# Performance work log

Hardware: AMD Instinct MI355X
Metric: run time of the kernel (lower is better)

Reference implementation:

```python
import jax, jax.numpy as jnp
import numpy as np

N_NODES = 500_000
N_EDGES = 8_000_000
W_PDE, W_BC, W_J1, W_J2 = 1.0, 100.0, 10.0, 10.0
EPS = 1e-8


def setup_inputs() -> dict:
    key = jax.random.key(0)
    ks = jax.random.split(key, 12)
    inp = {
        "u_pred": jax.random.normal(ks[0], (N_NODES, 1), jnp.float32),
        "x": jax.random.normal(ks[1], (N_NODES, 4), jnp.float32),
        # positions in [-1, 1] so the |pos|>0.99 boundary mask is nonempty
        "pos": 2.0 * jax.random.uniform(ks[2], (N_NODES, 2), jnp.float32) - 1.0,
        "y": jax.random.normal(ks[3], (N_NODES, 1), jnp.float32),
        "source": jax.random.normal(ks[4], (N_NODES, 1), jnp.float32),
        "j1": jax.random.normal(ks[5], (N_NODES, 1), jnp.float32),
        "coeff_dx": jax.random.normal(ks[6], (N_EDGES,), jnp.float32),
        "coeff_dy": jax.random.normal(ks[7], (N_EDGES,), jnp.float32),
        "coeff_lap": jax.random.normal(ks[8], (N_EDGES,), jnp.float32),
        "a": jnp.array([0.8], jnp.float32),
        "b": jnp.array([0.6], jnp.float32),
        "c": jnp.array([0.5], jnp.float32),
        "beta_minus": jnp.array([1.0], jnp.float32),
        "beta_plus": jnp.array([10.0], jnp.float32),
        "edge_index": jax.random.randint(ks[9], (2, N_EDGES), 0, N_NODES, jnp.int32),
        "edge_attr": jax.random.randint(ks[10], (N_EDGES,), 0, 2, jnp.int32),
    }
    return inp


def _masked_mean(sq, mask):
    # mean of sq over entries where mask is True (count>=1 guard, jit-safe)
    cnt = jnp.maximum(jnp.sum(mask.astype(sq.dtype)), 1.0)
    return jnp.sum(jnp.where(mask[:, None], sq, 0.0)) / cnt


def reference(u_pred, x, pos, y, source, j1, coeff_dx, coeff_dy, coeff_lap,
              a, b, c, beta_minus, beta_plus, edge_index, edge_attr):
    N = u_pred.shape[0]
    row, col = edge_index[0], edge_index[1]
    # GFD stencil derivatives: scatter-add of weighted differences over edges
    u_diff = u_pred[col] - u_pred[row]                       # [E,1]
    dx = jax.ops.segment_sum(u_diff * coeff_dx[:, None], row, num_segments=N)
    dy = jax.ops.segment_sum(u_diff * coeff_dy[:, None], row, num_segments=N)
    lap = jax.ops.segment_sum(u_diff * coeff_lap[:, None], row, num_segments=N)

    z = x[:, 3:4]                                            # [N,1]
    beta = jnp.where(z < 0, beta_minus, beta_plus)           # [N,1]
    res_pde = -lap - source / beta
    loss_pde = jnp.mean(res_pde ** 2)

    mask_bnd = (jnp.abs(pos[:, 0]) > 0.99) | (jnp.abs(pos[:, 1]) > 0.99)  # [N]
    loss_bc = _masked_mean((u_pred - y) ** 2, mask_bnd)

    # Interface (heterogeneous) edges
    m_het = edge_attr == 1                                   # [E]
    src, dst = row, col
    sign = jnp.sign(z[dst])                                  # [E,1]
    val_jump_pred = sign * (u_pred[dst] - u_pred[src])
    loss_j1 = _masked_mean((val_jump_pred - j1[src]) ** 2, m_het)

    # Elliptic interface normal at edge midpoints
    pos_mid = 0.5 * (pos[src] + pos[dst])                    # [E,2]
    nx = pos_mid[:, 0] / a ** 2
    ny = pos_mid[:, 1] / b ** 2
    nrm = jnp.maximum(jnp.sqrt(nx ** 2 + ny ** 2), EPS)      # [E]
    nxu, nyu = (nx / nrm)[:, None], (ny / nrm)[:, None]
    dn_src = dx[src] * nxu + dy[src] * nyu
    dn_dst = dx[dst] * nxu + dy[dst] * nyu
    flux_jump_pred = sign * (beta[dst] * dn_dst - beta[src] * dn_src)
    target_j2 = (2.0 * nrm * (c * beta_plus - beta_minus))[:, None]
    loss_j2 = _masked_mean((flux_jump_pred - target_j2) ** 2, m_het)

    loss_jump = W_J1 * loss_j1 + W_J2 * loss_j2
    total_loss = W_PDE * loss_pde + W_BC * loss_bc + loss_jump
    return total_loss
```

## Files before the change

kernel.cpp:

```cpp
#include <hip/hip_runtime.h>
#include <hip/hip_fp16.h>

#define N_NODES 500000
#define N_EDGES 8000000
#define EPSF 1e-8f

#define WIN_SHIFT 11
#define WINDOW 2048
#define NB 245
#define CHUNK 2000
#define NQ (CHUNK / 4)
#define NCHUNK 4000
#define SC_ITEMS 16

typedef int            v4i __attribute__((ext_vector_type(4)));
typedef float          v4f __attribute__((ext_vector_type(4)));
typedef unsigned short v4h __attribute__((ext_vector_type(4)));
typedef int            v2i __attribute__((ext_vector_type(2)));

struct Accum { double pde_sum, bc_sum, bc_cnt, j1_sum, j2_sum, het_cnt; };

__device__ __forceinline__ unsigned short f2h(float f) {
    return __half_as_ushort(__float2half(f));
}
__device__ __forceinline__ float h2f(unsigned short u) {
    return __half2float(__ushort_as_half(u));
}

__device__ double block_reduce(double v) {
    __shared__ double sm[16];
    __syncthreads();
    for (int off = 32; off; off >>= 1) v += __shfl_down(v, off, 64);
    const int lane = threadIdx.x & 63, wid = threadIdx.x >> 6;
    if (lane == 0) sm[wid] = v;
    __syncthreads();
    if (wid == 0) {
        const int nw = blockDim.x >> 6;
        v = (lane < nw) ? sm[lane] : 0.0;
        for (int off = 8; off; off >>= 1) v += __shfl_down(v, off, 64);
    }
    return v;
}

__device__ unsigned int block_excl_scan_u32(unsigned int x, unsigned int* smw) {
    const int lane = threadIdx.x & 63, wid = threadIdx.x >> 6;
    unsigned int v = x;
    for (int d = 1; d < 64; d <<= 1) {
        unsigned int t = __shfl_up(v, d, 64);
        if (lane >= d) v += t;
    }
    if (lane == 63) smw[wid] = v;
    __syncthreads();
    unsigned int base = 0;
    for (int w = 0; w < wid; ++w) base += smw[w];
    return base + v - x;
}

__global__ void prep(const float* __restrict__ x, const float* __restrict__ u,
                     const float* __restrict__ j1,
                     unsigned int* __restrict__ Tsrc, unsigned int* __restrict__ Tdst,
                     unsigned short* __restrict__ szh) {
    const int stride = gridDim.x * blockDim.x;
    for (int i = blockIdx.x * blockDim.x + threadIdx.x; i < N_NODES; i += stride) {
        const float z = x[4 * i + 3];
        const unsigned int uhb = f2h(u[i]);
        const unsigned short sb = f2h((float)(z > 0.f) - (float)(z < 0.f));
        Tsrc[i] = uhb | ((unsigned int)f2h(j1[i]) << 16);
        Tdst[i] = uhb | ((unsigned int)sb << 16);
        szh[i]  = sb;
    }
}

__global__ void k_hist(const v4i* __restrict__ row4, const v4i* __restrict__ attr4,
                       unsigned int* __restrict__ histC,
                       unsigned int* __restrict__ hist_het) {
    __shared__ unsigned int h[NB];
    __shared__ unsigned int hh;
    for (int i = threadIdx.x; i < NB; i += blockDim.x) h[i] = 0;
    if (threadIdx.x == 0) hh = 0;
    __syncthreads();
    const int ch = blockIdx.x;
    unsigned int my = 0;
    for (int q = threadIdx.x; q < NQ; q += blockDim.x) {
        const v4i r = __builtin_nontemporal_load(&row4[ch * NQ + q]);
        const v4i a = __builtin_nontemporal_load(&attr4[ch * NQ + q]);
        atomicAdd(&h[r[0] >> WIN_SHIFT], 1u);
        atomicAdd(&h[r[1] >> WIN_SHIFT], 1u);
        atomicAdd(&h[r[2] >> WIN_SHIFT], 1u);
        atomicAdd(&h[r[3] >> WIN_SHIFT], 1u);
        my += (a[0] == 1) + (a[1] == 1) + (a[2] == 1) + (a[3] == 1);
    }
    if (my) atomicAdd(&hh, my);
    __syncthreads();
    for (int i = threadIdx.x; i < NB; i += blockDim.x)
        histC[(size_t)ch * NB + i] = h[i];
    if (threadIdx.x == 0) hist_het[ch] = hh;
}

__global__ void k_scan1(const unsigned int* __restrict__ histC,
                        unsigned int* __restrict__ scannedB,
                        unsigned int* __restrict__ total) {
    __shared__ unsigned int v[NCHUNK];
    __shared__ unsigned int smw[4];
    const int b = blockIdx.x;
    for (int i = threadIdx.x; i < NCHUNK; i += blockDim.x)
        v[i] = histC[(size_t)i * NB + b];
    __syncthreads();
    const int i0 = threadIdx.x * SC_ITEMS;
    unsigned int s = 0;
    for (int k = 0; k < SC_ITEMS; ++k) { const int i = i0 + k; if (i < NCHUNK) s += v[i]; }
    const unsigned int ex = block_excl_scan_u32(s, smw);
    if (threadIdx.x == blockDim.x - 1) {
        total[b] = ex + s;
        scannedB[(size_t)b * (NCHUNK + 1) + NCHUNK] = ex + s;
    }
    unsigned int run = ex;
    for (int k = 0; k < SC_ITEMS; ++k) {
        const int i = i0 + k;
        if (i < NCHUNK) { scannedB[(size_t)b * (NCHUNK + 1) + i] = run; run += v[i]; }
    }
}

__global__ void k_scanhet(const unsigned int* __restrict__ hist_het,
                          unsigned int* __restrict__ hetbase) {
    __shared__ unsigned int v[NCHUNK];
    __shared__ unsigned int smw[4];
    for (int i = threadIdx.x; i < NCHUNK; i += blockDim.x) v[i] = hist_het[i];
    __syncthreads();
    const int i0 = threadIdx.x * SC_ITEMS;
    unsigned int s = 0;
    for (int k = 0; k < SC_ITEMS; ++k) { const int i = i0 + k; if (i < NCHUNK) s += v[i]; }
    const unsigned int ex = block_excl_scan_u32(s, smw);
    if (threadIdx.x == blockDim.x - 1) hetbase[NCHUNK] = ex + s;
    unsigned int run = ex;
    for (int k = 0; k < SC_ITEMS; ++k) {
        const int i = i0 + k;
        if (i < NCHUNK) { hetbase[i] = run; run += v[i]; }
    }
}

__global__ void k_tr(const unsigned int* __restrict__ in, unsigned int* __restrict__ out) {
    __shared__ unsigned int t[32][33];
    const int ch0 = blockIdx.x * 32, b0 = blockIdx.y * 32;
    const int tx = threadIdx.x & 31, ty0 = threadIdx.x >> 5;
    for (int j = ty0; j < 32; j += 8) {
        const int b = b0 + j, ch = ch0 + tx;
        if (b < NB && ch < NCHUNK + 1) t[j][tx] = in[(size_t)b * (NCHUNK + 1) + ch];
    }
    __syncthreads();
    for (int j = ty0; j < 32; j += 8) {
        const int ch = ch0 + j, b = b0 + tx;
        if (ch < NCHUNK + 1 && b < NB) out[(size_t)ch * NB + b] = t[tx][j];
    }
}

__global__ void k_scan2(const unsigned int* __restrict__ total, unsigned int* __restrict__ baseb) {
    __shared__ unsigned int smw[4];
    const unsigned int x = (threadIdx.x < NB) ? total[threadIdx.x] : 0;
    const unsigned int ex = block_excl_scan_u32(x, smw);
    if (threadIdx.x < NB) baseb[threadIdx.x] = ex;
}

template<int EMIT_HET>
__global__ void __launch_bounds__(256, 7)
k_scatter(const v4i* __restrict__ row4, const v4i* __restrict__ col4,
          const v4i* __restrict__ attr4,
          const v4f* __restrict__ cdx4, const v4f* __restrict__ cdy4,
          const v4f* __restrict__ clap4,
          const unsigned int* __restrict__ Tsrc, const unsigned int* __restrict__ Tdst,
          const unsigned int* __restrict__ baseb,
          const unsigned int* __restrict__ scannedC,
          const unsigned int* __restrict__ hetbase,
          v4h* __restrict__ rec, v2i* __restrict__ het, Accum* __restrict__ acc) {
    __shared__ int           lcur[NB];
    __shared__ unsigned int  lbase[NB];
    __shared__ unsigned int  gdest[NB];
    __shared__ unsigned int  smw[4];
    __shared__ v4h           o4[CHUNK];
    __shared__ unsigned char obk[CHUNK];
    __shared__ int           hcur;

    const int ch = blockIdx.x;
    unsigned int cnt = 0;
    if (threadIdx.x < NB) {
        const unsigned int s0 = scannedC[(size_t)ch * NB + threadIdx.x];
        const unsigned int s1 = scannedC[(size_t)(ch + 1) * NB + threadIdx.x];
        cnt = s1 - s0;
        gdest[threadIdx.x] = baseb[threadIdx.x] + s0;
        lcur[threadIdx.x] = 0;
    }
    if (EMIT_HET && threadIdx.x == 0) hcur = (int)hetbase[ch];
    const unsigned int exv = block_excl_scan_u32(cnt, smw);
    if (threadIdx.x < NB) lbase[threadIdx.x] = exv;
    __syncthreads();

    double j1s = 0.0;
    int hc = 0;
    for (int q = threadIdx.x; q < NQ; q += blockDim.x) {
        const v4i r4 = __builtin_nontemporal_load(&row4[ch * NQ + q]);
        const v4i c4 = __builtin_nontemporal_load(&col4[ch * NQ + q]);
        const v4i a4 = __builtin_nontemporal_load(&attr4[ch * NQ + q]);
        const v4f cx = __builtin_nontemporal_load(&cdx4[ch * NQ + q]);
        const v4f cy = __builtin_nontemporal_load(&cdy4[ch * NQ + q]);
        const v4f cl = __builtin_nontemporal_load(&clap4[ch * NQ + q]);
#pragma unroll
        for (int k = 0; k < 4; ++k) {
            const int r = r4[k], c = c4[k];
            const unsigned int ts = Tsrc[r];
            const unsigned int td = Tdst[c];
            const float ud = h2f((unsigned short)td) - h2f((unsigned short)ts);
            const int b = r >> WIN_SHIFT;
            const int p = (int)lbase[b] + atomicAdd(&lcur[b], 1);
            v4h rc;
            rc[0] = (unsigned short)(r & (WINDOW - 1));
            rc[1] = f2h(ud * cx[k]);
            rc[2] = f2h(ud * cy[k]);
            rc[3] = f2h(ud * cl[k]);
            o4[p] = rc;
            obk[p] = (unsigned char)b;
            if (a4[k] == 1) {
                const float d = h2f((unsigned short)(td >> 16)) * ud -
                                h2f((unsigned short)(ts >> 16));
                j1s += (double)(d * d);
                hc++;
                if (EMIT_HET) {
                    const int pos = atomicAdd(&hcur, 1);
                    v2i e; e[0] = r; e[1] = c;
                    __builtin_nontemporal_store(e, &het[pos]);
                }
            }
        }
    }
    __syncthreads();

    for (int i = threadIdx.x; i < CHUNK; i += blockDim.x) {
        const v4h rc = o4[i];
        const int b = obk[i];
        const unsigned int dest = gdest[b] + (unsigned int)(i - (int)lbase[b]);
        __builtin_nontemporal_store(rc, &rec[dest]);
    }

    double t = block_reduce(j1s);
    if (threadIdx.x == 0) atomicAdd(&acc->j1_sum, t);
    t = block_reduce((double)hc);
    if (threadIdx.x == 0) atomicAdd(&acc->het_cnt, t);
}

__global__ void k_acc(const v4h* __restrict__ rec,
                      const unsigned int* __restrict__ baseb,
                      const unsigned int* __restrict__ total,
                      const float* __restrict__ u, const unsigned short* __restrict__ szh,
                      const float2* __restrict__ pos2,
                      const float* __restrict__ y, const float* __restrict__ source,
                      const float* __restrict__ a_p, const float* __restrict__ b_p,
                      const float* __restrict__ bm_p, const float* __restrict__ bp_p,
                      v4h* __restrict__ Q, Accum* __restrict__ acc) {
    __shared__ float a3[WINDOW * 3];
    for (int i = threadIdx.x; i < WINDOW * 3; i += blockDim.x) a3[i] = 0.f;
    __syncthreads();
    const int b = blockIdx.x;
    const int s = (int)baseb[b];
    const int e = s + (int)total[b];
    for (int i = s + threadIdx.x; i < e; i += blockDim.x) {
        const v4h rc = __builtin_nontemporal_load(&rec[i]);
        const int lr = (int)(rc[0] & (WINDOW - 1)) * 3;
        atomicAdd(&a3[lr + 0], h2f(rc[1]));
        atomicAdd(&a3[lr + 1], h2f(rc[2]));
        atomicAdd(&a3[lr + 2], h2f(rc[3]));
    }
    __syncthreads();
    const float av = a_p[0], bv = b_p[0], bm = bm_p[0], bp = bp_p[0];
    const float ha = 0.5f / (av * av), hb = 0.5f / (bv * bv);
    double pde = 0.0, bcs = 0.0;
    int bcc = 0;
    const int n0 = b << WIN_SHIFT;
    const int n1 = min(n0 + WINDOW, N_NODES);
    for (int i = n0 + threadIdx.x; i < n1; i += blockDim.x) {
        const int l = (i - n0) * 3;
        const float szv = h2f(szh[i]);
        const float beta = (szv < 0.f) ? bm : bp;
        const float2 p = pos2[i];
        v4h qo;
        qo[0] = f2h(p.x * ha);
        qo[1] = f2h(p.y * hb);
        qo[2] = (unsigned short)((f2h(beta * a3[l]) & 0xFFFEu) | (szv < 0.f ? 1u : 0u));
        qo[3] = (unsigned short)((f2h(beta * a3[l + 1]) & 0xFFFEu) | (szv == 0.f ? 1u : 0u));
        Q[i] = qo;
        const float res = -a3[l + 2] - source[i] / beta;
        pde += (double)(res * res);
        if (fabsf(p.x) > 0.99f || fabsf(p.y) > 0.99f) {
            const float d = u[i] - y[i];
            bcs += (double)(d * d);
            bcc++;
        }
    }
    double t = block_reduce(pde);
    if (threadIdx.x == 0) atomicAdd(&acc->pde_sum, t);
    t = block_reduce(bcs);
    if (threadIdx.x == 0) atomicAdd(&acc->bc_sum, t);
    t = block_reduce((double)bcc);
    if (threadIdx.x == 0) atomicAdd(&acc->bc_cnt, t);
}

__global__ void k_pass2c(const v2i* __restrict__ het,
                         const unsigned int* __restrict__ hetbase,
                         const v4h* __restrict__ Q,
                         const float* __restrict__ c_p,
                         const float* __restrict__ bm_p, const float* __restrict__ bp_p,
                         Accum* __restrict__ acc) {
    const float tgt = 2.f * (c_p[0] * bp_p[0] - bm_p[0]);
    const int tot = (int)hetbase[NCHUNK];
    double j2s = 0.0;
    const int stride = gridDim.x * blockDim.x;
    for (int i = blockIdx.x * blockDim.x + threadIdx.x; i < tot; i += stride) {
        const v2i e = __builtin_nontemporal_load(&het[i]);
        const v4h qr = Q[e[0]];
        const v4h qc = Q[e[1]];
        const float nx = h2f(qr[0]) + h2f(qc[0]);
        const float ny = h2f(qr[1]) + h2f(qc[1]);
        const float nrm = fmaxf(sqrtf(nx * nx + ny * ny), EPSF);
        const float B = ((h2f(qc[2]) - h2f(qr[2])) * nx +
                         (h2f(qc[3]) - h2f(qr[3])) * ny) / nrm;
        const float sz = (qc[3] & 1u) ? 0.f : ((qc[2] & 1u) ? -1.f : 1.f);
        const float d = sz * B - tgt * nrm;
        j2s += (double)(d * d);
    }
    const double t = block_reduce(j2s);
    if (threadIdx.x == 0) atomicAdd(&acc->j2_sum, t);
}

__global__ void k_pass2(const v4i* __restrict__ row4, const v4i* __restrict__ col4,
                        const v4i* __restrict__ attr4,
                        const v4h* __restrict__ Q, const unsigned short* __restrict__ szh,
                        const float* __restrict__ c_p,
                        const float* __restrict__ bm_p, const float* __restrict__ bp_p,
                        Accum* __restrict__ acc) {
    const float tgt = 2.f * (c_p[0] * bp_p[0] - bm_p[0]);
    double j2s = 0.0;
    const int stride = gridDim.x * blockDim.x;
    const int NQT = N_EDGES / 4;
    for (int q = blockIdx.x * blockDim.x + threadIdx.x; q < NQT; q += stride) {
        const v4i r4 = __builtin_nontemporal_load(&row4[q]);
        const v4i c4 = __builtin_nontemporal_load(&col4[q]);
        const v4i a4 = __builtin_nontemporal_load(&attr4[q]);
#pragma unroll
        for (int k = 0; k < 4; ++k) {
            if (a4[k] != 1) continue;
            const int r = r4[k], c = c4[k];
            const v4h qr = Q[r];
            const v4h qc = Q[c];
            const float nx = h2f(qr[0]) + h2f(qc[0]);
            const float ny = h2f(qr[1]) + h2f(qc[1]);
            const float nrm = fmaxf(sqrtf(nx * nx + ny * ny), EPSF);
            const float B = ((h2f(qc[2]) - h2f(qr[2])) * nx +
                             (h2f(qc[3]) - h2f(qr[3])) * ny) / nrm;
            const float d = h2f(szh[c]) * B - tgt * nrm;
            j2s += (double)(d * d);
        }
    }
    const double t = block_reduce(j2s);
    if (threadIdx.x == 0) atomicAdd(&acc->j2_sum, t);
}

__global__ void fb_edge1(const unsigned int* __restrict__ Tsrc,
                         const unsigned int* __restrict__ Tdst,
                         const float* __restrict__ cdx, const float* __restrict__ cdy,
                         const float* __restrict__ clap,
                         const int* __restrict__ row, const int* __restrict__ col,
                         const int* __restrict__ attr,
                         float* __restrict__ rep, Accum* __restrict__ acc) {
    double j1s = 0.0;
    int hc = 0;
    const int stride = gridDim.x * blockDim.x;
    for (int e = blockIdx.x * blockDim.x + threadIdx.x; e < N_EDGES; e += stride) {
        const int r = row[e], c = col[e];
        const unsigned int ts = Tsrc[r];
        const unsigned int td = Tdst[c];
        const float ud = h2f((unsigned short)td) - h2f((unsigned short)ts);
        atomicAdd(&rep[4 * (size_t)r + 0], ud * cdx[e]);
        atomicAdd(&rep[4 * (size_t)r + 1], ud * cdy[e]);
        atomicAdd(&rep[4 * (size_t)r + 2], ud * clap[e]);
        if (attr[e] == 1) {
            const float d = h2f((unsigned short)(td >> 16)) * ud -
                            h2f((unsigned short)(ts >> 16));
            j1s += (double)(d * d);
            hc++;
        }
    }
    double t = block_reduce(j1s);
    if (threadIdx.x == 0) atomicAdd(&acc->j1_sum, t);
    t = block_reduce((double)hc);
    if (threadIdx.x == 0) atomicAdd(&acc->het_cnt, t);
}

__global__ void fb_reduce(const float4* __restrict__ rep,
                          const float* __restrict__ u, const unsigned short* __restrict__ szh,
                          const float2* __restrict__ pos2,
                          const float* __restrict__ y, const float* __restrict__ source,
                          const float* __restrict__ a_p, const float* __restrict__ b_p,
                          const float* __restrict__ bm_p, const float* __restrict__ bp_p,
                          v4h* __restrict__ Q, Accum* __restrict__ acc) {
    const float av = a_p[0], bv = b_p[0], bm = bm_p[0], bp = bp_p[0];
    const float ha = 0.5f / (av * av), hb = 0.5f / (bv * bv);
    double pde = 0.0, bcs = 0.0;
    int bcc = 0;
    const int stride = gridDim.x * blockDim.x;
    for (int i = blockIdx.x * blockDim.x + threadIdx.x; i < N_NODES; i += stride) {
        const float4 v = rep[i];
        const float szv = h2f(szh[i]);
        const float beta = (szv < 0.f) ? bm : bp;
        const float2 p = pos2[i];
        v4h qo;
        qo[0] = f2h(p.x * ha);
        qo[1] = f2h(p.y * hb);
        qo[2] = (unsigned short)((f2h(beta * v.x) & 0xFFFEu) | (szv < 0.f ? 1u : 0u));
        qo[3] = (unsigned short)((f2h(beta * v.y) & 0xFFFEu) | (szv == 0.f ? 1u : 0u));
        Q[i] = qo;
        const float res = -v.z - source[i] / beta;
        pde += (double)(res * res);
        if (fabsf(p.x) > 0.99f || fabsf(p.y) > 0.99f) {
            const float d = u[i] - y[i];
            bcs += (double)(d * d);
            bcc++;
        }
    }
    double t = block_reduce(pde);
    if (threadIdx.x == 0) atomicAdd(&acc->pde_sum, t);
    t = block_reduce(bcs);
    if (threadIdx.x == 0) atomicAdd(&acc->bc_sum, t);
    t = block_reduce((double)bcc);
    if (threadIdx.x == 0) atomicAdd(&acc->bc_cnt, t);
}

__global__ void finalize(const Accum* __restrict__ acc, float* __restrict__ out) {
    if (threadIdx.x == 0 && blockIdx.x == 0) {
        const double loss_pde = acc->pde_sum / (double)N_NODES;
        const double loss_bc  = acc->bc_sum / fmax(acc->bc_cnt, 1.0);
        const double hc       = fmax(acc->het_cnt, 1.0);
        out[0] = (float)(loss_pde + 100.0 * loss_bc +
                         10.0 * (acc->j1_sum / hc) + 10.0 * (acc->j2_sum / hc));
    }
}

extern "C" void kernel_launch(void* const* d_in, const int* in_sizes, int n_in,
                              void* d_out, int out_size, void* d_ws, size_t ws_size,
                              hipStream_t stream) {
    const float* u_pred = (const float*)d_in[0];
    const float* x      = (const float*)d_in[1];
    const float2* pos2  = (const float2*)d_in[2];
    const float* y      = (const float*)d_in[3];
    const float* source = (const float*)d_in[4];
    const float* j1v    = (const float*)d_in[5];
    const float* cdx    = (const float*)d_in[6];
    const float* cdy    = (const float*)d_in[7];
    const float* clap   = (const float*)d_in[8];
    const float* a_p    = (const float*)d_in[9];
    const float* b_p    = (const float*)d_in[10];
    const float* c_p    = (const float*)d_in[11];
    const float* bm_p   = (const float*)d_in[12];
    const float* bp_p   = (const float*)d_in[13];
    const int* row_idx  = (const int*)d_in[14];
    const int* col_idx  = row_idx + N_EDGES;
    const int* eattr    = (const int*)d_in[15];

    char* base_p = (char*)d_ws;
    size_t off = 0;
    auto alloc = [&](size_t bytes) { void* p = base_p + off; off = (off + bytes + 63) & ~(size_t)63; return p; };

    Accum* acc = (Accum*)alloc(sizeof(Accum));
    unsigned int* Tsrc = (unsigned int*)alloc((size_t)N_NODES * 4);
    unsigned int* Tdst = (unsigned int*)alloc((size_t)N_NODES * 4);
    unsigned short* szh = (unsigned short*)alloc((size_t)N_NODES * 2);
    v4h* Q = (v4h*)alloc((size_t)N_NODES * 8);
    unsigned int* histC    = (unsigned int*)alloc((size_t)(NCHUNK + 1) * NB * 4);
    unsigned int* scannedB = (unsigned int*)alloc((size_t)NB * (NCHUNK + 1) * 4);
    unsigned int* total    = (unsigned int*)alloc(NB * 4);
    unsigned int* baseb    = (unsigned int*)alloc(NB * 4);
    unsigned int* hist_het = (unsigned int*)alloc((size_t)NCHUNK * 4);
    unsigned int* hetbase  = (unsigned int*)alloc((size_t)(NCHUNK + 1) * 4);
    unsigned int* scannedC = histC;
    const size_t misc_end = off;
    v4h* rec = (v4h*)alloc((size_t)N_EDGES * 8);
    const size_t need_sort = off;
    v2i* het = (v2i*)alloc((size_t)N_EDGES * 8);
    const size_t need_het = off;

    const int threads = 256;
    const int nblocks = (N_NODES + threads - 1) / threads;

    hipMemsetAsync(d_ws, 0, 64, stream);
    prep<<<nblocks, threads, 0, stream>>>(x, u_pred, j1v, Tsrc, Tdst, szh);

    if (ws_size >= need_sort) {
        const bool emit = (ws_size >= need_het);
        k_hist<<<NCHUNK, threads, 0, stream>>>((const v4i*)row_idx, (const v4i*)eattr,
                                               histC, hist_het);
        k_scan1<<<NB, threads, 0, stream>>>(histC, scannedB, total);
        k_scanhet<<<1, threads, 0, stream>>>(hist_het, hetbase);
        {
            dim3 g((NCHUNK + 1 + 31) / 32, (NB + 31) / 32);
            k_tr<<<g, 256, 0, stream>>>(scannedB, scannedC);
        }
        k_scan2<<<1, threads, 0, stream>>>(total, baseb);
        if (emit) {
            k_scatter<1><<<NCHUNK, threads, 0, stream>>>(
                (const v4i*)row_idx, (const v4i*)col_idx, (const v4i*)eattr,
                (const v4f*)cdx, (const v4f*)cdy, (const v4f*)clap,
                Tsrc, Tdst, baseb, scannedC, hetbase, rec, het, acc);
        } else {
            k_scatter<0><<<NCHUNK, threads, 0, stream>>>(
                (const v4i*)row_idx, (const v4i*)col_idx, (const v4i*)eattr,
                (const v4f*)cdx, (const v4f*)cdy, (const v4f*)clap,
                Tsrc, Tdst, baseb, scannedC, hetbase, rec, het, acc);
        }
        k_acc<<<NB, threads, 0, stream>>>(rec, baseb, total, u_pred, szh, pos2, y, source,
                                          a_p, b_p, bm_p, bp_p, Q, acc);
        if (emit) {
            k_pass2c<<<1024, threads, 0, stream>>>(het, hetbase, Q, c_p, bm_p, bp_p, acc);
        } else {
            k_pass2<<<2048, threads, 0, stream>>>((const v4i*)row_idx, (const v4i*)col_idx,
                                                  (const v4i*)eattr, Q, szh,
                                                  c_p, bm_p, bp_p, acc);
        }
    } else {
        float4* rep = (float4*)(base_p + misc_end);
        hipMemsetAsync(rep, 0, (size_t)N_NODES * 16, stream);
        fb_edge1<<<2048, threads, 0, stream>>>(Tsrc, Tdst, cdx, cdy, clap,
                                               row_idx, col_idx, eattr, (float*)rep, acc);
        fb_reduce<<<nblocks, threads, 0, stream>>>(rep, u_pred, szh, pos2, y, source,
                                                   a_p, b_p, bm_p, bp_p, Q, acc);
        k_pass2<<<2048, threads, 0, stream>>>((const v4i*)row_idx, (const v4i*)col_idx,
                                              (const v4i*)eattr, Q, szh,
                                              c_p, bm_p, bp_p, acc);
    }

    finalize<<<1, 64, 0, stream>>>(acc, (float*)d_out);
}
```

Measured before the change: 429.3 us.

## Defer row-side gather and j1 loss to windowed accumulate kernel via LDS

```diff
diff --git a/kernel.cpp b/kernel.cpp
--- a/kernel.cpp
+++ b/kernel.cpp
@@ -57,17 +57,13 @@
 }
 
 __global__ void prep(const float* __restrict__ x, const float* __restrict__ u,
-                     const float* __restrict__ j1,
-                     unsigned int* __restrict__ Tsrc, unsigned int* __restrict__ Tdst,
-                     unsigned short* __restrict__ szh) {
+                     unsigned int* __restrict__ G, unsigned short* __restrict__ szh) {
     const int stride = gridDim.x * blockDim.x;
     for (int i = blockIdx.x * blockDim.x + threadIdx.x; i < N_NODES; i += stride) {
         const float z = x[4 * i + 3];
-        const unsigned int uhb = f2h(u[i]);
-        const unsigned short sb = f2h((float)(z > 0.f) - (float)(z < 0.f));
-        Tsrc[i] = uhb | ((unsigned int)f2h(j1[i]) << 16);
-        Tdst[i] = uhb | ((unsigned int)sb << 16);
-        szh[i]  = sb;
+        const unsigned int sz2 = (z < 0.f) ? 1u : ((z > 0.f) ? 0u : 2u);
+        G[i] = (unsigned int)f2h(u[i]) | (sz2 << 16);
+        szh[i] = f2h((float)(z > 0.f) - (float)(z < 0.f));
     }
 }
 
@@ -162,21 +158,23 @@
 }
 
 template<int EMIT_HET>
-__global__ void __launch_bounds__(256, 7)
+__global__ void __launch_bounds__(256, 6)
 k_scatter(const v4i* __restrict__ row4, const v4i* __restrict__ col4,
           const v4i* __restrict__ attr4,
           const v4f* __restrict__ cdx4, const v4f* __restrict__ cdy4,
           const v4f* __restrict__ clap4,
-          const unsigned int* __restrict__ Tsrc, const unsigned int* __restrict__ Tdst,
+          const unsigned int* __restrict__ G,
           const unsigned int* __restrict__ baseb,
           const unsigned int* __restrict__ scannedC,
           const unsigned int* __restrict__ hetbase,
-          v4h* __restrict__ rec, v2i* __restrict__ het, Accum* __restrict__ acc) {
+          v4h* __restrict__ rec8, unsigned short* __restrict__ recl,
+          v2i* __restrict__ het) {
     __shared__ int           lcur[NB];
     __shared__ unsigned int  lbase[NB];
     __shared__ unsigned int  gdest[NB];
     __shared__ unsigned int  smw[4];
     __shared__ v4h           o4[CHUNK];
+    __shared__ unsigned short oclap[CHUNK];
     __shared__ unsigned char obk[CHUNK];
     __shared__ int           hcur;
 
@@ -194,8 +192,6 @@
     if (threadIdx.x < NB) lbase[threadIdx.x] = exv;
     __syncthreads();
 
-    double j1s = 0.0;
-    int hc = 0;
     for (int q = threadIdx.x; q < NQ; q += blockDim.x) {
         const v4i r4 = __builtin_nontemporal_load(&row4[ch * NQ + q]);
         const v4i c4 = __builtin_nontemporal_load(&col4[ch * NQ + q]);
@@ -206,75 +202,87 @@
 #pragma unroll
         for (int k = 0; k < 4; ++k) {
             const int r = r4[k], c = c4[k];
-            const unsigned int ts = Tsrc[r];
-            const unsigned int td = Tdst[c];
-            const float ud = h2f((unsigned short)td) - h2f((unsigned short)ts);
+            const unsigned int g = G[c];
+            const unsigned int isHet = (a4[k] == 1) ? 1u : 0u;
             const int b = r >> WIN_SHIFT;
             const int p = (int)lbase[b] + atomicAdd(&lcur[b], 1);
             v4h rc;
-            rc[0] = (unsigned short)(r & (WINDOW - 1));
-            rc[1] = f2h(ud * cx[k]);
-            rc[2] = f2h(ud * cy[k]);
-            rc[3] = f2h(ud * cl[k]);
+            rc[0] = (unsigned short)((r & (WINDOW - 1)) | ((g >> 16) << 11) | (isHet << 13));
+            rc[1] = (unsigned short)(g & 0xFFFFu);
+            rc[2] = f2h(cx[k]);
+            rc[3] = f2h(cy[k]);
             o4[p] = rc;
+            oclap[p] = f2h(cl[k]);
             obk[p] = (unsigned char)b;
-            if (a4[k] == 1) {
-                const float d = h2f((unsigned short)(td >> 16)) * ud -
-                                h2f((unsigned short)(ts >> 16));
-                j1s += (double)(d * d);
-                hc++;
-                if (EMIT_HET) {
-                    const int pos = atomicAdd(&hcur, 1);
-                    v2i e; e[0] = r; e[1] = c;
-                    __builtin_nontemporal_store(e, &het[pos]);
-                }
+            if (EMIT_HET && isHet) {
+                const int pos = atomicAdd(&hcur, 1);
+                v2i e; e[0] = r; e[1] = c;
+                __builtin_nontemporal_store(e, &het[pos]);
             }
         }
     }
     __syncthreads();
 
     for (int i = threadIdx.x; i < CHUNK; i += blockDim.x) {
-        const v4h rc = o4[i];
         const int b = obk[i];
         const unsigned int dest = gdest[b] + (unsigned int)(i - (int)lbase[b]);
-        __builtin_nontemporal_store(rc, &rec[dest]);
-    }
-
-    double t = block_reduce(j1s);
-    if (threadIdx.x == 0) atomicAdd(&acc->j1_sum, t);
-    t = block_reduce((double)hc);
-    if (threadIdx.x == 0) atomicAdd(&acc->het_cnt, t);
-}
-
-__global__ void k_acc(const v4h* __restrict__ rec,
-                      const unsigned int* __restrict__ baseb,
-                      const unsigned int* __restrict__ total,
-                      const float* __restrict__ u, const unsigned short* __restrict__ szh,
-                      const float2* __restrict__ pos2,
-                      const float* __restrict__ y, const float* __restrict__ source,
-                      const float* __restrict__ a_p, const float* __restrict__ b_p,
-                      const float* __restrict__ bm_p, const float* __restrict__ bp_p,
-                      v4h* __restrict__ Q, Accum* __restrict__ acc) {
+        __builtin_nontemporal_store(o4[i], &rec8[dest]);
+        __builtin_nontemporal_store(oclap[i], &recl[dest]);
+    }
+}
+
+__global__ void __launch_bounds__(1024, 1)
+k_acc(const v4h* __restrict__ rec8, const unsigned short* __restrict__ recl,
+      const unsigned int* __restrict__ baseb,
+      const unsigned int* __restrict__ total,
+      const float* __restrict__ u, const float* __restrict__ j1v,
+      const unsigned short* __restrict__ szh,
+      const float2* __restrict__ pos2,
+      const float* __restrict__ y, const float* __restrict__ source,
+      const float* __restrict__ a_p, const float* __restrict__ b_p,
+      const float* __restrict__ bm_p, const float* __restrict__ bp_p,
+      v4h* __restrict__ Q, Accum* __restrict__ acc) {
     __shared__ float a3[WINDOW * 3];
+    __shared__ unsigned short u_lds[WINDOW];
+    __shared__ float j1_lds[WINDOW];
+    const int b = blockIdx.x;
+    const int n0 = b << WIN_SHIFT;
+    const int n1 = min(n0 + WINDOW, N_NODES);
     for (int i = threadIdx.x; i < WINDOW * 3; i += blockDim.x) a3[i] = 0.f;
-    __syncthreads();
-    const int b = blockIdx.x;
+    for (int i = threadIdx.x; i < WINDOW; i += blockDim.x) {
+        const int n = n0 + i;
+        u_lds[i]  = (n < N_NODES) ? f2h(u[n]) : 0;
+        j1_lds[i] = (n < N_NODES) ? j1v[n] : 0.f;
+    }
+    __syncthreads();
+
+    double j1s = 0.0;
+    int hc = 0;
     const int s = (int)baseb[b];
     const int e = s + (int)total[b];
     for (int i = s + threadIdx.x; i < e; i += blockDim.x) {
-        const v4h rc = __builtin_nontemporal_load(&rec[i]);
-        const int lr = (int)(rc[0] & (WINDOW - 1)) * 3;
-        atomicAdd(&a3[lr + 0], h2f(rc[1]));
-        atomicAdd(&a3[lr + 1], h2f(rc[2]));
-        atomicAdd(&a3[lr + 2], h2f(rc[3]));
-    }
-    __syncthreads();
+        const v4h rc = __builtin_nontemporal_load(&rec8[i]);
+        const unsigned short rl = __builtin_nontemporal_load(&recl[i]);
+        const unsigned int w0 = rc[0];
+        const int lr = (int)(w0 & (WINDOW - 1));
+        const float ud = h2f(rc[1]) - h2f(u_lds[lr]);
+        atomicAdd(&a3[lr * 3 + 0], ud * h2f(rc[2]));
+        atomicAdd(&a3[lr * 3 + 1], ud * h2f(rc[3]));
+        atomicAdd(&a3[lr * 3 + 2], ud * h2f(rl));
+        if (w0 & (1u << 13)) {
+            const unsigned int sz2 = (w0 >> 11) & 3u;
+            const float szc = (sz2 == 1u) ? -1.f : ((sz2 == 2u) ? 0.f : 1.f);
+            const float d = szc * ud - j1_lds[lr];
+            j1s += (double)(d * d);
+            hc++;
+        }
+    }
+    __syncthreads();
+
     const float av = a_p[0], bv = b_p[0], bm = bm_p[0], bp = bp_p[0];
     const float ha = 0.5f / (av * av), hb = 0.5f / (bv * bv);
     double pde = 0.0, bcs = 0.0;
     int bcc = 0;
-    const int n0 = b << WIN_SHIFT;
-    const int n1 = min(n0 + WINDOW, N_NODES);
     for (int i = n0 + threadIdx.x; i < n1; i += blockDim.x) {
         const int l = (i - n0) * 3;
         const float szv = h2f(szh[i]);
@@ -294,7 +302,11 @@
             bcc++;
         }
     }
-    double t = block_reduce(pde);
+    double t = block_reduce(j1s);
+    if (threadIdx.x == 0) atomicAdd(&acc->j1_sum, t);
+    t = block_reduce((double)hc);
+    if (threadIdx.x == 0) atomicAdd(&acc->het_cnt, t);
+    t = block_reduce(pde);
     if (threadIdx.x == 0) atomicAdd(&acc->pde_sum, t);
     t = block_reduce(bcs);
     if (threadIdx.x == 0) atomicAdd(&acc->bc_sum, t);
@@ -362,8 +374,8 @@
     if (threadIdx.x == 0) atomicAdd(&acc->j2_sum, t);
 }
 
-__global__ void fb_edge1(const unsigned int* __restrict__ Tsrc,
-                         const unsigned int* __restrict__ Tdst,
+__global__ void fb_edge1(const unsigned int* __restrict__ G,
+                         const float* __restrict__ j1v,
                          const float* __restrict__ cdx, const float* __restrict__ cdy,
                          const float* __restrict__ clap,
                          const int* __restrict__ row, const int* __restrict__ col,
@@ -374,15 +386,16 @@
     const int stride = gridDim.x * blockDim.x;
     for (int e = blockIdx.x * blockDim.x + threadIdx.x; e < N_EDGES; e += stride) {
         const int r = row[e], c = col[e];
-        const unsigned int ts = Tsrc[r];
-        const unsigned int td = Tdst[c];
-        const float ud = h2f((unsigned short)td) - h2f((unsigned short)ts);
+        const unsigned int gr = G[r];
+        const unsigned int gc = G[c];
+        const float ud = h2f((unsigned short)gc) - h2f((unsigned short)gr);
         atomicAdd(&rep[4 * (size_t)r + 0], ud * cdx[e]);
         atomicAdd(&rep[4 * (size_t)r + 1], ud * cdy[e]);
         atomicAdd(&rep[4 * (size_t)r + 2], ud * clap[e]);
         if (attr[e] == 1) {
-            const float d = h2f((unsigned short)(td >> 16)) * ud -
-                            h2f((unsigned short)(ts >> 16));
+            const unsigned int sz2 = gc >> 16;
+            const float szc = (sz2 == 1u) ? -1.f : ((sz2 == 2u) ? 0.f : 1.f);
+            const float d = szc * ud - j1v[r];
             j1s += (double)(d * d);
             hc++;
         }
@@ -468,8 +481,7 @@
     auto alloc = [&](size_t bytes) { void* p = base_p + off; off = (off + bytes + 63) & ~(size_t)63; return p; };
 
     Accum* acc = (Accum*)alloc(sizeof(Accum));
-    unsigned int* Tsrc = (unsigned int*)alloc((size_t)N_NODES * 4);
-    unsigned int* Tdst = (unsigned int*)alloc((size_t)N_NODES * 4);
+    unsigned int* G = (unsigned int*)alloc((size_t)N_NODES * 4);
     unsigned short* szh = (unsigned short*)alloc((size_t)N_NODES * 2);
     v4h* Q = (v4h*)alloc((size_t)N_NODES * 8);
     unsigned int* histC    = (unsigned int*)alloc((size_t)(NCHUNK + 1) * NB * 4);
@@ -480,7 +492,8 @@
     unsigned int* hetbase  = (unsigned int*)alloc((size_t)(NCHUNK + 1) * 4);
     unsigned int* scannedC = histC;
     const size_t misc_end = off;
-    v4h* rec = (v4h*)alloc((size_t)N_EDGES * 8);
+    v4h* rec8 = (v4h*)alloc((size_t)N_EDGES * 8);
+    unsigned short* recl = (unsigned short*)alloc((size_t)N_EDGES * 2);
     const size_t need_sort = off;
     v2i* het = (v2i*)alloc((size_t)N_EDGES * 8);
     const size_t need_het = off;
@@ -489,7 +502,7 @@
     const int nblocks = (N_NODES + threads - 1) / threads;
 
     hipMemsetAsync(d_ws, 0, 64, stream);
-    prep<<<nblocks, threads, 0, stream>>>(x, u_pred, j1v, Tsrc, Tdst, szh);
+    prep<<<nblocks, threads, 0, stream>>>(x, u_pred, G, szh);
 
     if (ws_size >= need_sort) {
         const bool emit = (ws_size >= need_het);
@@ -506,15 +519,15 @@
             k_scatter<1><<<NCHUNK, threads, 0, stream>>>(
                 (const v4i*)row_idx, (const v4i*)col_idx, (const v4i*)eattr,
                 (const v4f*)cdx, (const v4f*)cdy, (const v4f*)clap,
-                Tsrc, Tdst, baseb, scannedC, hetbase, rec, het, acc);
+                G, baseb, scannedC, hetbase, rec8, recl, het);
         } else {
             k_scatter<0><<<NCHUNK, threads, 0, stream>>>(
                 (const v4i*)row_idx, (const v4i*)col_idx, (const v4i*)eattr,
                 (const v4f*)cdx, (const v4f*)cdy, (const v4f*)clap,
-                Tsrc, Tdst, baseb, scannedC, hetbase, rec, het, acc);
-        }
-        k_acc<<<NB, threads, 0, stream>>>(rec, baseb, total, u_pred, szh, pos2, y, source,
-                                          a_p, b_p, bm_p, bp_p, Q, acc);
+                G, baseb, scannedC, hetbase, rec8, recl, het);
+        }
+        k_acc<<<NB, 1024, 0, stream>>>(rec8, recl, baseb, total, u_pred, j1v, szh,
+                                       pos2, y, source, a_p, b_p, bm_p, bp_p, Q, acc);
         if (emit) {
             k_pass2c<<<1024, threads, 0, stream>>>(het, hetbase, Q, c_p, bm_p, bp_p, acc);
         } else {
@@ -525,7 +538,7 @@
     } else {
         float4* rep = (float4*)(base_p + misc_end);
         hipMemsetAsync(rep, 0, (size_t)N_NODES * 16, stream);
-        fb_edge1<<<2048, threads, 0, stream>>>(Tsrc, Tdst, cdx, cdy, clap,
+        fb_edge1<<<2048, threads, 0, stream>>>(G, j1v, cdx, cdy, clap,
                                                row_idx, col_idx, eattr, (float*)rep, acc);
         fb_reduce<<<nblocks, threads, 0, stream>>>(rep, u_pred, szh, pos2, y, source,
                                                    a_p, b_p, bm_p, bp_p, Q, acc);
```

After: 440.4 us. 2.6% more time.
